# Kernel optimization log

Hardware: AMD Instinct MI355X
Metric: run time of the kernel (lower is better)

Reference implementation:

```python
import jax, jax.numpy as jnp
import numpy as np

LENGTH_OF_SIGNAL = 2560
OUTLIER_THRESHOLD = 3.0


def setup_inputs() -> dict:
    key = jax.random.key(0)
    inputs = jax.random.normal(key, (16384, 2560, 1), dtype=jnp.float32)
    return {"inputs": inputs}


def reference(inputs):
    # inputs: (B, S, 1). All stats reduce over the sequence axis (dim=1).
    B, S, _ = inputs.shape
    x = inputs[..., 0]  # (B, S)

    mean = jnp.mean(x, axis=1)                       # (B,)
    maximum = jnp.max(x, axis=1)
    minimum = jnp.min(x, axis=1)
    p2p = maximum - minimum
    rms = jnp.sqrt(jnp.mean(x * x, axis=1))
    var = jnp.var(x, axis=1, ddof=1)                 # torch.var is unbiased
    std = jnp.sqrt(var)                              # torch.std is unbiased

    centered = x - mean[:, None]
    skewness = jnp.mean(centered ** 3, axis=1) / (std ** 3)
    kurtosis = jnp.mean(centered ** 4, axis=1) / (std ** 4)

    abs_x = jnp.abs(x)
    abs_sum = jnp.sum(abs_x, axis=1)
    abs_max = jnp.max(abs_x, axis=1)
    shape_factor = rms * LENGTH_OF_SIGNAL / abs_sum
    impulse_factor = abs_max * LENGTH_OF_SIGNAL / abs_sum

    outliers = jnp.sum(
        (jnp.abs(centered) > OUTLIER_THRESHOLD * std[:, None]).astype(jnp.int32),
        axis=1,
    ).astype(jnp.float32)

    # zero-crossing rate on flattened (B, S) signal
    zcr = jnp.sum(
        (jnp.diff(jnp.sign(x), axis=1) != 0).astype(jnp.float32), axis=1
    ) / (2.0 * S)

    # Hjorth parameters (activity, mobility, complexity)
    d1 = jnp.diff(x, axis=1)
    d2 = jnp.diff(d1, axis=1)
    var_d1 = jnp.var(d1, axis=1, ddof=1)
    var_d2 = jnp.var(d2, axis=1, ddof=1)
    activity = var
    mobility = jnp.sqrt(var_d1 / var)
    complexity = jnp.sqrt(var_d2 / var_d1)

    stacked = jnp.stack(
        [mean, maximum, minimum, p2p, var, rms, skewness, kurtosis,
         shape_factor, impulse_factor, outliers, zcr,
         activity, mobility, complexity],
        axis=1,
    )  # (B, 15)
    return stacked
```

## Files before the change

kernel.cpp:

```cpp
#include <hip/hip_runtime.h>
#include <math.h>


typedef float f32x2 __attribute__((ext_vector_type(2)));
typedef float f32x4 __attribute__((ext_vector_type(4)));

constexpr int S_LEN = 2560;
constexpr int NROWS = 16384;

#define DPP_ADD_F32(x, ctrl) do { \
    int t_ = __builtin_amdgcn_update_dpp(0, __float_as_int(x), ctrl, 0xf, 0xf, false); \
    x += __int_as_float(t_); } while (0)
#define DPP_MAX_F32(x, ctrl) do { \
    int t_ = __builtin_amdgcn_update_dpp(__float_as_int(x), __float_as_int(x), ctrl, 0xf, 0xf, false); \
    x = fmaxf(x, __int_as_float(t_)); } while (0)
#define DPP_MIN_F32(x, ctrl) do { \
    int t_ = __builtin_amdgcn_update_dpp(__float_as_int(x), __float_as_int(x), ctrl, 0xf, 0xf, false); \
    x = fminf(x, __int_as_float(t_)); } while (0)

__device__ __forceinline__ float wave_sum_f32(float x) {
    DPP_ADD_F32(x, 0x111); DPP_ADD_F32(x, 0x112); DPP_ADD_F32(x, 0x114);
    DPP_ADD_F32(x, 0x118); DPP_ADD_F32(x, 0x142); DPP_ADD_F32(x, 0x143);
    return x;
}
__device__ __forceinline__ float wave_max_f32(float x) {
    DPP_MAX_F32(x, 0x111); DPP_MAX_F32(x, 0x112); DPP_MAX_F32(x, 0x114);
    DPP_MAX_F32(x, 0x118); DPP_MAX_F32(x, 0x142); DPP_MAX_F32(x, 0x143);
    return x;
}
__device__ __forceinline__ float wave_min_f32(float x) {
    DPP_MIN_F32(x, 0x111); DPP_MIN_F32(x, 0x112); DPP_MIN_F32(x, 0x114);
    DPP_MIN_F32(x, 0x118); DPP_MIN_F32(x, 0x142); DPP_MIN_F32(x, 0x143);
    return x;
}
__device__ __forceinline__ double wave_sum_f64(double x) {
#define DPP_ADD_F64(ctrl) do { \
    long long b_ = __double_as_longlong(x); \
    int lo_ = __builtin_amdgcn_update_dpp(0, (int)(b_ & 0xffffffffLL), ctrl, 0xf, 0xf, false); \
    int hi_ = __builtin_amdgcn_update_dpp(0, (int)(b_ >> 32), ctrl, 0xf, 0xf, false); \
    x += __longlong_as_double(((long long)hi_ << 32) | (unsigned int)lo_); } while (0)
    DPP_ADD_F64(0x111); DPP_ADD_F64(0x112); DPP_ADD_F64(0x114);
    DPP_ADD_F64(0x118); DPP_ADD_F64(0x142); DPP_ADD_F64(0x143);
#undef DPP_ADD_F64
    return x;
}
__device__ __forceinline__ double readlane_f64(double x, int l) {
    long long b = __double_as_longlong(x);
    int lo = __builtin_amdgcn_readlane((int)(b & 0xffffffffLL), l);
    int hi = __builtin_amdgcn_readlane((int)(b >> 32), l);
    return __longlong_as_double(((long long)hi << 32) | (unsigned int)lo);
}

__global__ __launch_bounds__(256, 6)
void health_pass1(const float* __restrict__ in, float* __restrict__ ws) {
    __shared__ double Lsum[4], Lsq[4];
    __shared__ float  Lnb[2][2];

    const int lane = threadIdx.x & 63;
    const int wid  = threadIdx.x >> 6;
    const int hidx = wid & 1;
    const int rsl  = wid >> 1;
    const int row  = blockIdx.x * 2 + rsl;

    const f32x4* rp = reinterpret_cast<const f32x4*>(in)
                    + (size_t)row * (S_LEN / 4) + hidx * (1280 / 4) + lane;

    f32x4 X[5];
#pragma unroll
    for (int k = 0; k < 5; ++k) X[k] = rp[k * 64];

    f32x2 sp = {0.f, 0.f}, qp = {0.f, 0.f};
    float sabs = 0.f, vmax = -INFINITY, vmin = INFINITY;
#pragma unroll
    for (int k = 0; k < 5; ++k) {
        f32x2 lo = __builtin_shufflevector(X[k], X[k], 0, 1);
        f32x2 hi = __builtin_shufflevector(X[k], X[k], 2, 3);
        sp += lo + hi;
        qp = __builtin_elementwise_fma(lo, lo, qp);
        qp = __builtin_elementwise_fma(hi, hi, qp);
        sabs += (fabsf(X[k][0]) + fabsf(X[k][1])) + (fabsf(X[k][2]) + fabsf(X[k][3]));
        vmax = fmaxf(fmaxf(X[k][2], X[k][3]), fmaxf(fmaxf(X[k][0], X[k][1]), vmax));
        vmin = fminf(fminf(X[k][2], X[k][3]), fminf(fminf(X[k][0], X[k][1]), vmin));
    }

    const double sum_l = (double)sp.x + (double)sp.y;
    const double sq_l  = (double)qp.x + (double)qp.y;
    const double sum_u = readlane_f64(wave_sum_f64(sum_l), 63);
    const double sq_u  = readlane_f64(wave_sum_f64(sq_l), 63);

    if (lane == 0) {
        Lsum[wid] = sum_u;  Lsq[wid] = sq_u;
        if (hidx == 1) { Lnb[rsl][0] = X[0][0]; Lnb[rsl][1] = X[0][1]; }
    }
    __syncthreads();
    const double tsum = Lsum[rsl * 2] + Lsum[rsl * 2 + 1];
    const double tsq  = Lsq[rsl * 2]  + Lsq[rsl * 2 + 1];

    const double mean = tsum * (1.0 / S_LEN);
    const double var  = (tsq - tsum * mean) * (1.0 / (S_LEN - 1));
    const double stdv = sqrt(var);
    const double thr  = 3.0 * stdv;
    const double bhi = mean + thr, blo = mean - thr;
    float bhi_f = (float)bhi;
    if ((double)bhi_f > bhi) bhi_f = __int_as_float(__float_as_int(bhi_f) - 1);
    float blo_f = (float)blo;
    if ((double)blo_f < blo) blo_f = __int_as_float(__float_as_int(blo_f) - 1);

    const float nbv0 = (hidx == 0) ? Lnb[rsl][0] : 0.f;
    const float nbv1 = (hidx == 0) ? Lnb[rsl][1] : 0.f;
    const float mf = (float)mean;
    const f32x2 nmf2 = {-mf, -mf};

    f32x2 c3p = {0.f, 0.f}, c4p = {0.f, 0.f};
    float r1 = 0.f, r2 = 0.f;
    int outc = 0, zcc = 0;
    const unsigned long long tail_ok = (hidx == 0) ? ~0ULL : 0x7FFFFFFFFFFFFFFFULL;

#pragma unroll
    for (int k = 0; k < 5; ++k) {
        const float x0 = X[k][0], x1 = X[k][1], x2v = X[k][2], x3 = X[k][3];
        const int kn = (k == 4) ? 0 : (k + 1);
        float v0 = (lane == 0) ? X[kn][0] : x0;
        float v1 = (lane == 0) ? X[kn][1] : x1;
        float n0 = __shfl(v0, (lane + 1) & 63);
        float n1 = __shfl(v1, (lane + 1) & 63);
        if (k == 4 && lane == 63) { n0 = nbv0; n1 = nbv1; }

        f32x2 lo = __builtin_shufflevector(X[k], X[k], 0, 1);
        f32x2 hi = __builtin_shufflevector(X[k], X[k], 2, 3);
        f32x2 cl = lo + nmf2, ch = hi + nmf2;
        f32x2 ql = cl * cl,  qh = ch * ch;
        c3p = __builtin_elementwise_fma(ql, cl, c3p);
        c3p = __builtin_elementwise_fma(qh, ch, c3p);
        c4p = __builtin_elementwise_fma(ql, ql, c4p);
        c4p = __builtin_elementwise_fma(qh, qh, c4p);

        outc += __popcll(__ballot(x0  > bhi_f || x0  < blo_f));
        outc += __popcll(__ballot(x1  > bhi_f || x1  < blo_f));
        outc += __popcll(__ballot(x2v > bhi_f || x2v < blo_f));
        outc += __popcll(__ballot(x3  > bhi_f || x3  < blo_f));

        const unsigned long long m0 = __ballot(x0  < 0.f);
        const unsigned long long m1 = __ballot(x1  < 0.f);
        const unsigned long long m2 = __ballot(x2v < 0.f);
        const unsigned long long m3 = __ballot(x3  < 0.f);
        const unsigned long long mn = __ballot(n0  < 0.f);
        zcc += __popcll(m0 ^ m1) + __popcll(m1 ^ m2) + __popcll(m2 ^ m3);
        zcc += __popcll((m3 ^ mn) & ((k == 4) ? tail_ok : ~0ULL));

        r1 = fmaf(x0, x1, fmaf(x1, x2v, fmaf(x2v, x3, fmaf(x3, n0, r1))));
        r2 = fmaf(x0, x2v, fmaf(x1, x3, fmaf(x2v, n0, fmaf(x3, n1, r2))));
    }

    float sabs_t = wave_sum_f32(sabs);
    float c3_t   = wave_sum_f32(c3p.x + c3p.y);
    float c4_t   = wave_sum_f32(c4p.x + c4p.y);
    float r1_t   = wave_sum_f32(r1);
    float r2_t   = wave_sum_f32(r2);
    float vmax_t = wave_max_f32(vmax);
    float vmin_t = wave_min_f32(vmin);

    float ep_a, ep_b;
    if (hidx == 0) {
        ep_a = __int_as_float(__builtin_amdgcn_readlane(__float_as_int(X[0][0]), 0));
        ep_b = __int_as_float(__builtin_amdgcn_readlane(__float_as_int(X[0][1]), 0));
    } else {
        ep_a = X[4][2];  ep_b = X[4][3];
    }

    if (lane == 63) {
        double2* Wd = reinterpret_cast<double2*>(ws);
        f32x4*   Wf = reinterpret_cast<f32x4*>(ws);
        double2 dsum; dsum.x = sum_u; dsum.y = sq_u;
        Wd[(size_t)hidx * NROWS + row] = dsum;
        const size_t b = (size_t)(2 + hidx * 3) * NROWS + row;
        Wf[b]             = f32x4{sabs_t, vmax_t, vmin_t, c3_t};
        Wf[b + NROWS]     = f32x4{c4_t, r1_t, r2_t, (float)outc};
        Wf[b + 2 * NROWS] = f32x4{(float)zcc, ep_a, ep_b, 0.f};
    }
}

__global__ __launch_bounds__(256)
void health_finalize(const float* __restrict__ ws, float* __restrict__ out) {
    const int row = blockIdx.x * 256 + threadIdx.x;
    const double2* Wd = reinterpret_cast<const double2*>(ws);
    const f32x4*   Wf = reinterpret_cast<const f32x4*>(ws);

    const double2 s0 = Wd[row], s1 = Wd[NROWS + row];
    const f32x4 a0 = Wf[2 * NROWS + row], a1 = Wf[3 * NROWS + row], a2 = Wf[4 * NROWS + row];
    const f32x4 b0 = Wf[5 * NROWS + row], b1 = Wf[6 * NROWS + row], b2 = Wf[7 * NROWS + row];

    const double tsum = s0.x + s1.x;
    const double tsq  = s0.y + s1.y;
    const double mean = tsum * (1.0 / S_LEN);
    const double var  = (tsq - tsum * mean) * (1.0 / (S_LEN - 1));
    const double stdv = sqrt(var);

    const float tabs = a0[0] + b0[0];
    const float tmax = fmaxf(a0[1], b0[1]);
    const float tmin = fminf(a0[2], b0[2]);
    const float c3t  = a0[3] + b0[3];
    const float c4t  = a1[0] + b1[0];
    const double r1t = (double)a1[1] + (double)b1[1];
    const double r2t = (double)a1[2] + (double)b1[2];
    const float outt = a1[3] + b1[3];
    const float zct  = a2[0] + b2[0];
    const double e0 = (double)a2[1], e1 = (double)a2[2];
    const double e2 = (double)b2[1], e3 = (double)b2[2];

    const double rms  = sqrt(tsq * (1.0 / S_LEN));
    const double m3   = (double)c3t * (1.0 / S_LEN);
    const double m4   = (double)c4t * (1.0 / S_LEN);
    const double skew = m3 / (var * stdv);
    const double kurt = m4 / (var * var);
    const float  amax = fmaxf(fabsf(tmax), fabsf(tmin));
    const double shape   = rms * (double)S_LEN / (double)tabs;
    const double impulse = (double)amax * (double)S_LEN / (double)tabs;

    const double Q = tsq;
    const double s1q = 2.0 * Q - 2.0 * r1t - e0 * e0 - e3 * e3;
    const double s2q = 6.0 * Q - 8.0 * r1t + 2.0 * r2t
                     + 4.0 * (e0 * e1 + e2 * e3)
                     - 5.0 * e0 * e0 - e1 * e1 - e2 * e2 - 5.0 * e3 * e3;
    const double sd1 = e3 - e0;
    const double sd2 = (e3 - e2) - (e1 - e0);
    const double var1 = (s1q - sd1 * sd1 * (1.0 / (S_LEN - 1))) * (1.0 / (S_LEN - 2));
    const double var2 = (s2q - sd2 * sd2 * (1.0 / (S_LEN - 2))) * (1.0 / (S_LEN - 3));

    float* o = out + (size_t)row * 15;
    o[0]  = (float)mean;
    o[1]  = tmax;
    o[2]  = tmin;
    o[3]  = tmax - tmin;
    o[4]  = (float)var;
    o[5]  = (float)rms;
    o[6]  = (float)skew;
    o[7]  = (float)kurt;
    o[8]  = (float)shape;
    o[9]  = (float)impulse;
    o[10] = outt;
    o[11] = zct * (1.0f / (2.0f * S_LEN));
    o[12] = (float)var;
    o[13] = (float)sqrt(var1 / var);
    o[14] = (float)sqrt(var2 / var1);
}

extern "C" void kernel_launch(void* const* d_in, const int* in_sizes, int n_in,
                              void* d_out, int out_size, void* d_ws, size_t ws_size,
                              hipStream_t stream) {
    (void)in_sizes; (void)n_in; (void)ws_size; (void)out_size;
    const float* in = (const float*)d_in[0];
    float* out = (float*)d_out;
    float* ws  = (float*)d_ws;
    health_pass1<<<8192, 256, 0, stream>>>(in, ws);
    health_finalize<<<64, 256, 0, stream>>>(ws, out);
}
```

Baseline: 36.69 us.

## Fuse finalize into single-wave-per-row stats kernel, drop workspace pass

```diff
diff --git a/kernel.cpp b/kernel.cpp
--- a/kernel.cpp
+++ b/kernel.cpp
@@ -6,7 +6,6 @@
 typedef float f32x4 __attribute__((ext_vector_type(4)));
 
 constexpr int S_LEN = 2560;
-constexpr int NROWS = 16384;
 
 #define DPP_ADD_F32(x, ctrl) do { \
     int t_ = __builtin_amdgcn_update_dpp(0, __float_as_int(x), ctrl, 0xf, 0xf, false); \
@@ -52,79 +51,77 @@
 }
 
 __global__ __launch_bounds__(256, 6)
-void health_pass1(const float* __restrict__ in, float* __restrict__ ws) {
-    __shared__ double Lsum[4], Lsq[4];
-    __shared__ float  Lnb[2][2];
-
+void health_stats(const float* __restrict__ in, float* __restrict__ out) {
     const int lane = threadIdx.x & 63;
     const int wid  = threadIdx.x >> 6;
-    const int hidx = wid & 1;
-    const int rsl  = wid >> 1;
-    const int row  = blockIdx.x * 2 + rsl;
+    const int row  = blockIdx.x * 4 + wid;
 
     const f32x4* rp = reinterpret_cast<const f32x4*>(in)
-                    + (size_t)row * (S_LEN / 4) + hidx * (1280 / 4) + lane;
-
-    f32x4 X[5];
+                    + (size_t)row * (S_LEN / 4) + lane;
+
+    f32x4 X[10];
 #pragma unroll
-    for (int k = 0; k < 5; ++k) X[k] = rp[k * 64];
-
-    f32x2 sp = {0.f, 0.f}, qp = {0.f, 0.f};
-    float sabs = 0.f, vmax = -INFINITY, vmin = INFINITY;
+    for (int k = 0; k < 10; ++k) X[k] = rp[k * 64];
+
+    const float ep0 = __int_as_float(__builtin_amdgcn_readlane(__float_as_int(X[0][0]), 0));
+    const float ep1 = __int_as_float(__builtin_amdgcn_readlane(__float_as_int(X[0][1]), 0));
+
+    f32x2 sp = {0.f, 0.f}, qp = {0.f, 0.f}, sabsp = {0.f, 0.f};
+    f32x2 vmaxp = {-INFINITY, -INFINITY}, vminp = {INFINITY, INFINITY};
 #pragma unroll
-    for (int k = 0; k < 5; ++k) {
+    for (int k = 0; k < 10; ++k) {
         f32x2 lo = __builtin_shufflevector(X[k], X[k], 0, 1);
         f32x2 hi = __builtin_shufflevector(X[k], X[k], 2, 3);
         sp += lo + hi;
         qp = __builtin_elementwise_fma(lo, lo, qp);
         qp = __builtin_elementwise_fma(hi, hi, qp);
-        sabs += (fabsf(X[k][0]) + fabsf(X[k][1])) + (fabsf(X[k][2]) + fabsf(X[k][3]));
-        vmax = fmaxf(fmaxf(X[k][2], X[k][3]), fmaxf(fmaxf(X[k][0], X[k][1]), vmax));
-        vmin = fminf(fminf(X[k][2], X[k][3]), fminf(fminf(X[k][0], X[k][1]), vmin));
+        sabsp += __builtin_elementwise_max(lo, -lo);
+        sabsp += __builtin_elementwise_max(hi, -hi);
+        vmaxp = __builtin_elementwise_max(vmaxp, __builtin_elementwise_max(lo, hi));
+        vminp = __builtin_elementwise_min(vminp, __builtin_elementwise_min(lo, hi));
     }
 
     const double sum_l = (double)sp.x + (double)sp.y;
     const double sq_l  = (double)qp.x + (double)qp.y;
-    const double sum_u = readlane_f64(wave_sum_f64(sum_l), 63);
-    const double sq_u  = readlane_f64(wave_sum_f64(sq_l), 63);
-
-    if (lane == 0) {
-        Lsum[wid] = sum_u;  Lsq[wid] = sq_u;
-        if (hidx == 1) { Lnb[rsl][0] = X[0][0]; Lnb[rsl][1] = X[0][1]; }
-    }
-    __syncthreads();
-    const double tsum = Lsum[rsl * 2] + Lsum[rsl * 2 + 1];
-    const double tsq  = Lsq[rsl * 2]  + Lsq[rsl * 2 + 1];
+    const double tsum = readlane_f64(wave_sum_f64(sum_l), 63);
+    const double tsq  = readlane_f64(wave_sum_f64(sq_l), 63);
+
+    float sabs_t = wave_sum_f32(sabsp.x + sabsp.y);
+    float vmax_t = wave_max_f32(fmaxf(vmaxp.x, vmaxp.y));
+    float vmin_t = wave_min_f32(fminf(vminp.x, vminp.y));
 
     const double mean = tsum * (1.0 / S_LEN);
     const double var  = (tsq - tsum * mean) * (1.0 / (S_LEN - 1));
     const double stdv = sqrt(var);
     const double thr  = 3.0 * stdv;
+
     const double bhi = mean + thr, blo = mean - thr;
     float bhi_f = (float)bhi;
     if ((double)bhi_f > bhi) bhi_f = __int_as_float(__float_as_int(bhi_f) - 1);
     float blo_f = (float)blo;
     if ((double)blo_f < blo) blo_f = __int_as_float(__float_as_int(blo_f) - 1);
 
-    const float nbv0 = (hidx == 0) ? Lnb[rsl][0] : 0.f;
-    const float nbv1 = (hidx == 0) ? Lnb[rsl][1] : 0.f;
     const float mf = (float)mean;
     const f32x2 nmf2 = {-mf, -mf};
+    const int nli = (lane + 1) & 63;
 
     f32x2 c3p = {0.f, 0.f}, c4p = {0.f, 0.f};
     float r1 = 0.f, r2 = 0.f;
     int outc = 0, zcc = 0;
-    const unsigned long long tail_ok = (hidx == 0) ? ~0ULL : 0x7FFFFFFFFFFFFFFFULL;
 
 #pragma unroll
-    for (int k = 0; k < 5; ++k) {
+    for (int k = 0; k < 10; ++k) {
         const float x0 = X[k][0], x1 = X[k][1], x2v = X[k][2], x3 = X[k][3];
-        const int kn = (k == 4) ? 0 : (k + 1);
-        float v0 = (lane == 0) ? X[kn][0] : x0;
-        float v1 = (lane == 0) ? X[kn][1] : x1;
-        float n0 = __shfl(v0, (lane + 1) & 63);
-        float n1 = __shfl(v1, (lane + 1) & 63);
-        if (k == 4 && lane == 63) { n0 = nbv0; n1 = nbv1; }
+        float v0, v1;
+        if (k < 9) {
+            v0 = (lane == 0) ? X[k + 1][0] : x0;
+            v1 = (lane == 0) ? X[k + 1][1] : x1;
+        } else {
+            v0 = (lane == 0) ? 0.f : x0;
+            v1 = (lane == 0) ? 0.f : x1;
+        }
+        const float n0 = __shfl(v0, nli);
+        const float n1 = __shfl(v1, nli);
 
         f32x2 lo = __builtin_shufflevector(X[k], X[k], 0, 1);
         f32x2 hi = __builtin_shufflevector(X[k], X[k], 2, 3);
@@ -146,112 +143,63 @@
         const unsigned long long m3 = __ballot(x3  < 0.f);
         const unsigned long long mn = __ballot(n0  < 0.f);
         zcc += __popcll(m0 ^ m1) + __popcll(m1 ^ m2) + __popcll(m2 ^ m3);
-        zcc += __popcll((m3 ^ mn) & ((k == 4) ? tail_ok : ~0ULL));
+        zcc += __popcll((m3 ^ mn) & ((k == 9) ? 0x7FFFFFFFFFFFFFFFULL : ~0ULL));
 
         r1 = fmaf(x0, x1, fmaf(x1, x2v, fmaf(x2v, x3, fmaf(x3, n0, r1))));
         r2 = fmaf(x0, x2v, fmaf(x1, x3, fmaf(x2v, n0, fmaf(x3, n1, r2))));
     }
 
-    float sabs_t = wave_sum_f32(sabs);
-    float c3_t   = wave_sum_f32(c3p.x + c3p.y);
-    float c4_t   = wave_sum_f32(c4p.x + c4p.y);
-    float r1_t   = wave_sum_f32(r1);
-    float r2_t   = wave_sum_f32(r2);
-    float vmax_t = wave_max_f32(vmax);
-    float vmin_t = wave_min_f32(vmin);
-
-    float ep_a, ep_b;
-    if (hidx == 0) {
-        ep_a = __int_as_float(__builtin_amdgcn_readlane(__float_as_int(X[0][0]), 0));
-        ep_b = __int_as_float(__builtin_amdgcn_readlane(__float_as_int(X[0][1]), 0));
-    } else {
-        ep_a = X[4][2];  ep_b = X[4][3];
+    const float c3_t = wave_sum_f32(c3p.x + c3p.y);
+    const float c4_t = wave_sum_f32(c4p.x + c4p.y);
+    const float r1_t = wave_sum_f32(r1);
+    const float r2_t = wave_sum_f32(r2);
+
+    if (lane == 63) {
+        const double rms  = sqrt(tsq * (1.0 / S_LEN));
+        const double m3d  = (double)c3_t * (1.0 / S_LEN);
+        const double m4d  = (double)c4_t * (1.0 / S_LEN);
+        const double skew = m3d / (var * stdv);
+        const double kurt = m4d / (var * var);
+        const float  amax = fmaxf(fabsf(vmax_t), fabsf(vmin_t));
+        const double shape   = rms * (double)S_LEN / (double)sabs_t;
+        const double impulse = (double)amax * (double)S_LEN / (double)sabs_t;
+
+        const double e0 = (double)ep0, e1 = (double)ep1;
+        const double e2 = (double)X[9][2], e3 = (double)X[9][3];
+        const double Q = tsq, r1d = (double)r1_t, r2d = (double)r2_t;
+        const double s1q = 2.0 * Q - 2.0 * r1d - e0 * e0 - e3 * e3;
+        const double s2q = 6.0 * Q - 8.0 * r1d + 2.0 * r2d
+                         + 4.0 * (e0 * e1 + e2 * e3)
+                         - 5.0 * e0 * e0 - e1 * e1 - e2 * e2 - 5.0 * e3 * e3;
+        const double sd1 = e3 - e0;
+        const double sd2 = (e3 - e2) - (e1 - e0);
+        const double var1 = (s1q - sd1 * sd1 * (1.0 / (S_LEN - 1))) * (1.0 / (S_LEN - 2));
+        const double var2 = (s2q - sd2 * sd2 * (1.0 / (S_LEN - 2))) * (1.0 / (S_LEN - 3));
+
+        float* o = out + (size_t)row * 15;
+        o[0]  = (float)mean;
+        o[1]  = vmax_t;
+        o[2]  = vmin_t;
+        o[3]  = vmax_t - vmin_t;
+        o[4]  = (float)var;
+        o[5]  = (float)rms;
+        o[6]  = (float)skew;
+        o[7]  = (float)kurt;
+        o[8]  = (float)shape;
+        o[9]  = (float)impulse;
+        o[10] = (float)outc;
+        o[11] = (float)zcc * (1.0f / (2.0f * S_LEN));
+        o[12] = (float)var;
+        o[13] = (float)sqrt(var1 / var);
+        o[14] = (float)sqrt(var2 / var1);
     }
-
-    if (lane == 63) {
-        double2* Wd = reinterpret_cast<double2*>(ws);
-        f32x4*   Wf = reinterpret_cast<f32x4*>(ws);
-        double2 dsum; dsum.x = sum_u; dsum.y = sq_u;
-        Wd[(size_t)hidx * NROWS + row] = dsum;
-        const size_t b = (size_t)(2 + hidx * 3) * NROWS + row;
-        Wf[b]             = f32x4{sabs_t, vmax_t, vmin_t, c3_t};
-        Wf[b + NROWS]     = f32x4{c4_t, r1_t, r2_t, (float)outc};
-        Wf[b + 2 * NROWS] = f32x4{(float)zcc, ep_a, ep_b, 0.f};
-    }
-}
-
-__global__ __launch_bounds__(256)
-void health_finalize(const float* __restrict__ ws, float* __restrict__ out) {
-    const int row = blockIdx.x * 256 + threadIdx.x;
-    const double2* Wd = reinterpret_cast<const double2*>(ws);
-    const f32x4*   Wf = reinterpret_cast<const f32x4*>(ws);
-
-    const double2 s0 = Wd[row], s1 = Wd[NROWS + row];
-    const f32x4 a0 = Wf[2 * NROWS + row], a1 = Wf[3 * NROWS + row], a2 = Wf[4 * NROWS + row];
-    const f32x4 b0 = Wf[5 * NROWS + row], b1 = Wf[6 * NROWS + row], b2 = Wf[7 * NROWS + row];
-
-    const double tsum = s0.x + s1.x;
-    const double tsq  = s0.y + s1.y;
-    const double mean = tsum * (1.0 / S_LEN);
-    const double var  = (tsq - tsum * mean) * (1.0 / (S_LEN - 1));
-    const double stdv = sqrt(var);
-
-    const float tabs = a0[0] + b0[0];
-    const float tmax = fmaxf(a0[1], b0[1]);
-    const float tmin = fminf(a0[2], b0[2]);
-    const float c3t  = a0[3] + b0[3];
-    const float c4t  = a1[0] + b1[0];
-    const double r1t = (double)a1[1] + (double)b1[1];
-    const double r2t = (double)a1[2] + (double)b1[2];
-    const float outt = a1[3] + b1[3];
-    const float zct  = a2[0] + b2[0];
-    const double e0 = (double)a2[1], e1 = (double)a2[2];
-    const double e2 = (double)b2[1], e3 = (double)b2[2];
-
-    const double rms  = sqrt(tsq * (1.0 / S_LEN));
-    const double m3   = (double)c3t * (1.0 / S_LEN);
-    const double m4   = (double)c4t * (1.0 / S_LEN);
-    const double skew = m3 / (var * stdv);
-    const double kurt = m4 / (var * var);
-    const float  amax = fmaxf(fabsf(tmax), fabsf(tmin));
-    const double shape   = rms * (double)S_LEN / (double)tabs;
-    const double impulse = (double)amax * (double)S_LEN / (double)tabs;
-
-    const double Q = tsq;
-    const double s1q = 2.0 * Q - 2.0 * r1t - e0 * e0 - e3 * e3;
-    const double s2q = 6.0 * Q - 8.0 * r1t + 2.0 * r2t
-                     + 4.0 * (e0 * e1 + e2 * e3)
-                     - 5.0 * e0 * e0 - e1 * e1 - e2 * e2 - 5.0 * e3 * e3;
-    const double sd1 = e3 - e0;
-    const double sd2 = (e3 - e2) - (e1 - e0);
-    const double var1 = (s1q - sd1 * sd1 * (1.0 / (S_LEN - 1))) * (1.0 / (S_LEN - 2));
-    const double var2 = (s2q - sd2 * sd2 * (1.0 / (S_LEN - 2))) * (1.0 / (S_LEN - 3));
-
-    float* o = out + (size_t)row * 15;
-    o[0]  = (float)mean;
-    o[1]  = tmax;
-    o[2]  = tmin;
-    o[3]  = tmax - tmin;
-    o[4]  = (float)var;
-    o[5]  = (float)rms;
-    o[6]  = (float)skew;
-    o[7]  = (float)kurt;
-    o[8]  = (float)shape;
-    o[9]  = (float)impulse;
-    o[10] = outt;
-    o[11] = zct * (1.0f / (2.0f * S_LEN));
-    o[12] = (float)var;
-    o[13] = (float)sqrt(var1 / var);
-    o[14] = (float)sqrt(var2 / var1);
 }
 
 extern "C" void kernel_launch(void* const* d_in, const int* in_sizes, int n_in,
                               void* d_out, int out_size, void* d_ws, size_t ws_size,
                               hipStream_t stream) {
-    (void)in_sizes; (void)n_in; (void)ws_size; (void)out_size;
+    (void)in_sizes; (void)n_in; (void)d_ws; (void)ws_size; (void)out_size;
     const float* in = (const float*)d_in[0];
     float* out = (float*)d_out;
-    float* ws  = (float*)d_ws;
-    health_pass1<<<8192, 256, 0, stream>>>(in, ws);
-    health_finalize<<<64, 256, 0, stream>>>(ws, out);
-}
+    health_stats<<<4096, 256, 0, stream>>>(in, out);
+}
```

Result: slower. 41.07 us (+11.9%).
